# Kernel optimization log

Measured on AMD Instinct MI355X. Metric: run time of the kernel, lower is better.

## Reference

```python
import jax, jax.numpy as jnp
import numpy as np
from jax import lax

B, C, H, W = 8, 256, 32, 32
HEADS = 8
NUM_OFF = 9
OFF_SCALE = 0.1


def setup_inputs() -> dict:
    key = jax.random.key(0)
    ks = jax.random.split(key, 8)
    f = lambda k, s, sc: jax.random.normal(k, s, dtype=jnp.float32) * sc
    return {
        'query_map': f(ks[0], (B, C, H, W), 1.0),
        'kv_map': f(ks[1], (B, C, H, W), 1.0),
        'Wq': f(ks[2], (C, C), C ** -0.5),
        'Wk': f(ks[3], (C, C), C ** -0.5),
        'Wv': f(ks[4], (C, C), C ** -0.5),
        'Woff1': f(ks[5], (C // 2, C, 3, 3), (C * 9) ** -0.5),
        'boff1': jnp.zeros((C // 2,), jnp.float32),
        'Woff2': f(ks[6], (NUM_OFF * 2, C // 2), (C // 2) ** -0.5),
        'boff2': jnp.zeros((NUM_OFF * 2,), jnp.float32),
        'Wout': f(ks[7], (C, C), C ** -0.5),
        'bout': jnp.zeros((C,), jnp.float32),
    }


def grid_sample_bilinear_border(img, grid):
    """img: (B,C,H,W); grid: (B,H,W,2) with (x,y) in [-1,1], align_corners=True,
    padding_mode='border'. Returns (B,C,H,W)."""
    Bn, Cn, Hn, Wn = img.shape
    x = (grid[..., 0] + 1.0) * 0.5 * (Wn - 1)
    y = (grid[..., 1] + 1.0) * 0.5 * (Hn - 1)
    # border padding: clamp continuous coords into the valid range
    x = jnp.clip(x, 0.0, Wn - 1)
    y = jnp.clip(y, 0.0, Hn - 1)
    x0 = jnp.floor(x)
    y0 = jnp.floor(y)
    wx = x - x0
    wy = y - y0
    x0i = x0.astype(jnp.int32)
    y0i = y0.astype(jnp.int32)
    x1i = jnp.minimum(x0i + 1, Wn - 1)
    y1i = jnp.minimum(y0i + 1, Hn - 1)
    flat = img.reshape(Bn, Cn, Hn * Wn)

    def gat(iy, ix):
        idx = (iy * Wn + ix).reshape(Bn, 1, -1)  # broadcasts over channels
        return jnp.take_along_axis(flat, idx, axis=2)

    v00 = gat(y0i, x0i)
    v01 = gat(y0i, x1i)
    v10 = gat(y1i, x0i)
    v11 = gat(y1i, x1i)
    wxf = wx.reshape(Bn, 1, -1)
    wyf = wy.reshape(Bn, 1, -1)
    out = (v00 * (1 - wxf) + v01 * wxf) * (1 - wyf) + (v10 * (1 - wxf) + v11 * wxf) * wyf
    return out.reshape(Bn, Cn, Hn, Wn)


def reference(query_map, kv_map, Wq, Wk, Wv, Woff1, boff1, Woff2, boff2, Wout, bout):
    Bn, Cn, Hn, Wn = query_map.shape
    hd = Cn // HEADS
    # 1x1 conv projections as channel einsums
    q = jnp.einsum('oc,bchw->bohw', Wq, query_map)
    # offset network: 3x3 conv -> relu -> 1x1 conv
    h1 = lax.conv_general_dilated(q, Woff1, (1, 1), 'SAME',
                                  dimension_numbers=('NCHW', 'OIHW', 'NCHW'))
    h1 = jax.nn.relu(h1 + boff1[None, :, None, None])
    offsets = jnp.einsum('oc,bchw->bohw', Woff2, h1) + boff2[None, :, None, None]
    offsets = offsets.reshape(Bn, NUM_OFF, 2, Hn, Wn)
    offset = offsets[:, 0] * OFF_SCALE  # (B,2,H,W); ch0 -> x, ch1 -> y
    # normalized base grid in [-1,1] (align_corners=True convention)
    gx = jnp.linspace(-1.0, 1.0, Wn, dtype=q.dtype)[None, :]  # (1,W)
    gy = jnp.linspace(-1.0, 1.0, Hn, dtype=q.dtype)[:, None]  # (H,1)
    vx = gx[None] + offset[:, 0]  # (B,H,W)
    vy = gy[None] + offset[:, 1]
    vgrid = jnp.stack([vx, vy], axis=-1)  # (B,H,W,2)
    kv_sampled = grid_sample_bilinear_border(kv_map, vgrid)
    k = jnp.einsum('oc,bchw->bohw', Wk, kv_sampled)
    v = jnp.einsum('oc,bchw->bohw', Wv, kv_sampled)
    # (B,C,H,W) -> (B,heads,HW,hd)
    def to_heads(t):
        return t.reshape(Bn, HEADS, hd, Hn * Wn).transpose(0, 1, 3, 2)
    qh, kh, vh = to_heads(q), to_heads(k), to_heads(v)
    scale = hd ** -0.5
    attn = jnp.einsum('bhqd,bhkd->bhqk', qh, kh) * scale
    attn = jax.nn.softmax(attn, axis=-1)
    out = jnp.einsum('bhqk,bhkd->bhqd', attn, vh)
    out = out.transpose(0, 1, 3, 2).reshape(Bn, Cn, Hn, Wn)
    out = jnp.einsum('oc,bchw->bohw', Wout, out) + bout[None, :, None, None]
    return out
```

## Files before the change

kernel.cpp:

```cpp
#include <hip/hip_runtime.h>

#define HW_ 1024

typedef __attribute__((ext_vector_type(8))) short bf16x8;
typedef __attribute__((ext_vector_type(4))) short bf16x4;
typedef __attribute__((ext_vector_type(4))) float f32x4;

__device__ inline unsigned short f2bf(float f) {
  unsigned int u = __float_as_uint(f);
  u += 0x7FFF + ((u >> 16) & 1);
  return (unsigned short)(u >> 16);
}
__device__ inline unsigned short f2bf_fast(float f) {
  return (unsigned short)((__float_as_uint(f) + 0x8000u) >> 16);
}
__device__ inline float bf2f(unsigned short h) {
  return __uint_as_float(((unsigned int)h) << 16);
}
__device__ inline void async_copy16(const void* g, void* l) {
  __builtin_amdgcn_global_load_lds(
      (const __attribute__((address_space(1))) unsigned int*)g,
      (__attribute__((address_space(3))) unsigned int*)l, 16, 0, 0);
}

__global__ __launch_bounds__(256) void prep(
    const float* __restrict__ kv,
    const float* __restrict__ Wq, const float* __restrict__ Wk,
    const float* __restrict__ Wv, const float* __restrict__ Wo,
    const float* __restrict__ Woff1,
    short* __restrict__ WH, short* __restrict__ WL, short* __restrict__ wb,
    float* __restrict__ kvT)
{
  __shared__ float T[256][33];
  const int bid = blockIdx.x, t = threadIdx.x;

  if (bid < 256) {
    int b = bid >> 5, p0 = (bid & 31) * 32;
    int pp = t & 31, cg = t >> 5;
#pragma unroll
    for (int i = 0; i < 32; ++i) {
      int c = cg * 32 + i;
      T[c][pp] = kv[((size_t)(b * 256 + c)) * HW_ + p0 + pp];
    }
    __syncthreads();
#pragma unroll
    for (int r = 0; r < 8; ++r) {
      int e = t + 256 * r;
      int c4 = (e & 63) * 4, pp2 = e >> 6;
      float4 v4;
      v4.x = T[c4 + 0][pp2];
      v4.y = T[c4 + 1][pp2];
      v4.z = T[c4 + 2][pp2];
      v4.w = T[c4 + 3][pp2];
      *(float4*)&kvT[((size_t)(b * 1024 + p0 + pp2)) * 256 + c4] = v4;
    }
  } else if (bid < 512) {
    int b2 = bid - 256;
    int mat = b2 >> 6;
    int loc = (b2 & 63) * 1024 + t * 4;
    const float* W = (mat == 0) ? Wq : (mat == 1) ? Wk : (mat == 2) ? Wv : Wo;
    float4 f4 = *(const float4*)&W[loc];
    float f[4] = {f4.x, f4.y, f4.z, f4.w};
    bf16x4 h4, l4;
#pragma unroll
    for (int j = 0; j < 4; ++j) {
      unsigned short h = f2bf(f[j]);
      h4[j] = (short)h;
      l4[j] = (short)f2bf(f[j] - bf2f(h));
    }
    int r = loc >> 8, c = loc & 255;
    int mtile = r >> 4, k0s = c >> 5;
    int lane_ = ((c >> 3) & 3) * 16 + (r & 15);
    int pidx = (((mtile * 8 + k0s) * 64 + lane_) * 8) + (c & 7);
    *(bf16x4*)&WH[mat * 65536 + pidx] = h4;
    *(bf16x4*)&WL[mat * 65536 + pidx] = l4;
  } else {
    int e0 = (bid - 512) * 1024 + t * 4;
    int c = e0 & 255;
    int o = (e0 >> 8) & 127;
    int tap = e0 >> 15;
    bf16x4 h4;
#pragma unroll
    for (int j = 0; j < 4; ++j)
      h4[j] = (short)f2bf(Woff1[((size_t)(o * 256 + c + j)) * 9 + tap]);
    int otile = o >> 4, c0s = c >> 5;
    int lane_ = ((c >> 3) & 3) * 16 + (o & 15);
    int widx = ((((tap * 8 + otile) * 8 + c0s) * 64 + lane_) * 8) + (c & 7);
    *(bf16x4*)&wb[widx] = h4;
  }
}

__global__ __launch_bounds__(256) void qgemm(
    const short* __restrict__ WH, const short* __restrict__ WL,
    const float* __restrict__ Xf,
    short* __restrict__ Yt, short* __restrict__ Yh2, short* __restrict__ Yl2)
{
  __shared__ short Bsh[32][40];
  __shared__ short Bsl[32][40];
  const int t    = threadIdx.x;
  const int w    = t >> 6;
  const int lane = t & 63;
  const int ln   = lane & 15;
  const int qd   = lane >> 4;
  const int bp0  = blockIdx.x * 32;
  const int mb   = blockIdx.y * 8 + w * 2;
  const int bB   = bp0 >> 10, p0l = bp0 & 1023;

  f32x4 acc[2][2] = {};
#pragma unroll
  for (int k0 = 0; k0 < 256; k0 += 32) {
    __syncthreads();
    {
      int pp = t & 31, cg = t >> 5;
      float fv[4];
#pragma unroll
      for (int j = 0; j < 4; ++j)
        fv[j] = Xf[((size_t)(bB * 256 + k0 + cg * 4 + j)) * HW_ + p0l + pp];
      bf16x4 h4, l4;
#pragma unroll
      for (int j = 0; j < 4; ++j) {
        unsigned short h = f2bf(fv[j]);
        h4[j] = (short)h;
        l4[j] = (short)f2bf(fv[j] - bf2f(h));
      }
      *(bf16x4*)&Bsh[pp][cg * 4] = h4;
      *(bf16x4*)&Bsl[pp][cg * 4] = l4;
    }
    __syncthreads();

    bf16x8 Ah[2], Al[2], Bh[2], Bl[2];
    const int k0s = k0 >> 5;
#pragma unroll
    for (int mt = 0; mt < 2; ++mt) {
      size_t wi = ((size_t)(((mb + mt) * 8 + k0s) * 64 + lane)) * 8;
      Ah[mt] = *(const bf16x8*)&WH[wi];
      Al[mt] = *(const bf16x8*)&WL[wi];
    }
#pragma unroll
    for (int nt = 0; nt < 2; ++nt) {
      Bh[nt] = *(const bf16x8*)&Bsh[nt * 16 + ln][qd * 8];
      Bl[nt] = *(const bf16x8*)&Bsl[nt * 16 + ln][qd * 8];
    }
#pragma unroll
    for (int mt = 0; mt < 2; ++mt)
#pragma unroll
      for (int nt = 0; nt < 2; ++nt) {
        acc[mt][nt] = __builtin_amdgcn_mfma_f32_16x16x32_bf16(Ah[mt], Bh[nt], acc[mt][nt], 0, 0, 0);
        acc[mt][nt] = __builtin_amdgcn_mfma_f32_16x16x32_bf16(Ah[mt], Bl[nt], acc[mt][nt], 0, 0, 0);
        acc[mt][nt] = __builtin_amdgcn_mfma_f32_16x16x32_bf16(Al[mt], Bh[nt], acc[mt][nt], 0, 0, 0);
      }
  }

  const int om = blockIdx.y * 128 + w * 32;
  const float sc = 0.25506063286f;
#pragma unroll
  for (int mt = 0; mt < 2; ++mt)
#pragma unroll
    for (int nt = 0; nt < 2; ++nt) {
      int bp = bp0 + nt * 16 + ln;
      int b = bp >> 10, p = bp & 1023;
#pragma unroll
      for (int i = 0; i < 4; ++i) {
        int o = om + mt * 16 + qd * 4 + i;
        int h = o >> 5, d = o & 31;
        Yt[(((size_t)(b * 8 + h)) * 1024 + p) * 32 + d] = (short)f2bf(acc[mt][nt][i] * sc);
      }
      int ob = om + mt * 16 + qd * 4;
      bf16x4 h4, l4;
#pragma unroll
      for (int i = 0; i < 4; ++i) {
        float f = acc[mt][nt][i];
        unsigned short h = f2bf(f);
        h4[i] = (short)h;
        l4[i] = (short)f2bf(f - bf2f(h));
      }
      *(bf16x4*)&Yh2[(size_t)bp * 256 + ob] = h4;
      *(bf16x4*)&Yl2[(size_t)bp * 256 + ob] = l4;
    }
}

__global__ __launch_bounds__(512) void convkv(
    const short* __restrict__ wb, const float* __restrict__ bias,
    const float* __restrict__ W2, const float* __restrict__ b2,
    const short* __restrict__ xh, const short* __restrict__ xl,
    const float* __restrict__ kvT,
    const short* __restrict__ WH, const short* __restrict__ WL,
    short* __restrict__ kt, short* __restrict__ vt)
{
  __shared__ short Xs[2][3][34][264];
  __shared__ short XsH[32][264];
  __shared__ short XsL[32][264];
  __shared__ float red[4][32][2];
  __shared__ float2 crd[32];
  const int id   = blockIdx.x;
  const int b    = id & 7;
  const int y0   = id >> 3;
  const int t    = threadIdx.x;
  const int w    = t >> 6;
  const int lane = t & 63;
  const int ln   = lane & 15;
  const int qd   = lane >> 4;
  const int bp0  = (b * 32 + y0) * 32;

  {
    bf16x8 v[12];
#pragma unroll
    for (int i = 0; i < 12; ++i) {
      int e = t + 512 * i;
      int oct = e & 31;
      int x   = (e >> 5) & 31;
      int rr  = e >> 10;
      int hl  = rr / 3, r = rr % 3;
      int yy  = y0 + r - 1;
      bf16x8 val = {};
      if (yy >= 0 && yy < 32) {
        const short* src = hl ? xl : xh;
        val = *(const bf16x8*)&src[((size_t)((b * 32 + yy) * 32 + x)) * 256 + oct * 8];
      }
      v[i] = val;
    }
#pragma unroll
    for (int i = 0; i < 12; ++i) {
      int e = t + 512 * i;
      int oct = e & 31;
      int x   = (e >> 5) & 31;
      int rr  = e >> 10;
      int hl  = rr / 3, r = rr % 3;
      *(bf16x8*)&Xs[hl][r][x + 1][oct * 8] = v[i];
    }
    if (t < 384) {
      int oct  = t & 31;
      int colw = (t >> 5) & 1;
      int rr   = t >> 6;
      int hl   = rr / 3, r = rr % 3;
      bf16x8 zz = {};
      *(bf16x8*)&Xs[hl][r][colw ? 33 : 0][oct * 8] = zz;
    }
  }
  __syncthreads();

  const int chh = w >> 2;
  const int ow  = w & 3;
  const int o0c = ow * 32;
  f32x4 acc[2][2] = {};
#pragma unroll
  for (int c0s = 0; c0s < 4; ++c0s) {
    const int c0 = chh * 128 + c0s * 32;
    const int c0abs = chh * 4 + c0s;
#pragma unroll
    for (int tap = 0; tap < 9; ++tap) {
      const int ky = tap / 3, kx = tap % 3;
      bf16x8 afr[2];
#pragma unroll
      for (int m = 0; m < 2; ++m)
        afr[m] = *(const bf16x8*)&wb[((((tap * 8 + (ow * 2 + m)) * 8 + c0abs) * 64
                                       + lane) * 8)];
#pragma unroll
      for (int nt = 0; nt < 2; ++nt) {
        int hc = nt * 16 + ln + kx;
        bf16x8 bh = *(const bf16x8*)&Xs[0][ky][hc][c0 + qd * 8];
        bf16x8 bl = *(const bf16x8*)&Xs[1][ky][hc][c0 + qd * 8];
#pragma unroll
        for (int m = 0; m < 2; ++m) {
          acc[m][nt] = __builtin_amdgcn_mfma_f32_16x16x32_bf16(afr[m], bh, acc[m][nt], 0, 0, 0);
          acc[m][nt] = __builtin_amdgcn_mfma_f32_16x16x32_bf16(afr[m], bl, acc[m][nt], 0, 0, 0);
        }
      }
    }
  }

  float* ps = (float*)&XsH[0][0];
  if (w >= 4) {
#pragma unroll
    for (int m = 0; m < 2; ++m)
#pragma unroll
      for (int nt = 0; nt < 2; ++nt)
        *(f32x4*)&ps[(((w - 4) * 64 + lane) * 4 + m * 2 + nt) * 4] = acc[m][nt];
  }
  __syncthreads();

  if (w < 4) {
    float ps0[2] = {0.f, 0.f}, ps1[2] = {0.f, 0.f};
#pragma unroll
    for (int m = 0; m < 2; ++m)
#pragma unroll
      for (int nt = 0; nt < 2; ++nt) {
        f32x4 p = *(const f32x4*)&ps[((w * 64 + lane) * 4 + m * 2 + nt) * 4];
        acc[m][nt] += p;
      }
#pragma unroll
    for (int m = 0; m < 2; ++m)
#pragma unroll
      for (int i = 0; i < 4; ++i) {
        int o = o0c + m * 16 + qd * 4 + i;
        float bo = bias[o];
        float w2a = W2[o], w2b = W2[128 + o];
#pragma unroll
        for (int nt = 0; nt < 2; ++nt) {
          float h = fmaxf(acc[m][nt][i] + bo, 0.f);
          ps0[nt] += w2a * h;
          ps1[nt] += w2b * h;
        }
      }
#pragma unroll
    for (int msk = 16; msk < 64; msk <<= 1) {
      ps0[0] += __shfl_xor(ps0[0], msk, 64);
      ps0[1] += __shfl_xor(ps0[1], msk, 64);
      ps1[0] += __shfl_xor(ps1[0], msk, 64);
      ps1[1] += __shfl_xor(ps1[1], msk, 64);
    }
    if (qd == 0) {
#pragma unroll
      for (int nt = 0; nt < 2; ++nt) {
        red[w][nt * 16 + ln][0] = ps0[nt];
        red[w][nt * 16 + ln][1] = ps1[nt];
      }
    }
  }
  __syncthreads();
  if (t < 32) {
    float c0s = (red[0][t][0] + red[1][t][0]) + (red[2][t][0] + red[3][t][0]) + b2[0];
    float c1s = (red[0][t][1] + red[1][t][1]) + (red[2][t][1] + red[3][t][1]) + b2[1];
    float gx = -1.f + 2.f * (float)t / 31.f;
    float gy = -1.f + 2.f * (float)y0 / 31.f;
    float vx = gx + 0.1f * c0s;
    float vy = gy + 0.1f * c1s;
    float px = fminf(fmaxf((vx + 1.f) * 0.5f * 31.f, 0.f), 31.f);
    float py = fminf(fmaxf((vy + 1.f) * 0.5f * 31.f, 0.f), 31.f);
    crd[t] = make_float2(px, py);
  }
  __syncthreads();

#pragma unroll
  for (int it = 0; it < 2; ++it) {
    int e = t + 512 * it;
    int oct = e & 31, row = e >> 5;
    float2 cd = crd[row];
    float x0f = floorf(cd.x), y0f = floorf(cd.y);
    float wx = cd.x - x0f, wy = cd.y - y0f;
    int x0 = (int)x0f, y0i = (int)y0f;
    int x1 = min(x0 + 1, 31), y1 = min(y0i + 1, 31);
    float w00 = (1.f - wx) * (1.f - wy), w01 = wx * (1.f - wy);
    float w10 = (1.f - wx) * wy,         w11 = wx * wy;
    const float* r00 = &kvT[((size_t)(b * 1024 + y0i * 32 + x0)) * 256 + oct * 8];
    const float* r01 = &kvT[((size_t)(b * 1024 + y0i * 32 + x1)) * 256 + oct * 8];
    const float* r10 = &kvT[((size_t)(b * 1024 + y1 * 32 + x0)) * 256 + oct * 8];
    const float* r11 = &kvT[((size_t)(b * 1024 + y1 * 32 + x1)) * 256 + oct * 8];
    float4 a00 = *(const float4*)r00, b00 = *(const float4*)(r00 + 4);
    float4 a01 = *(const float4*)r01, b01 = *(const float4*)(r01 + 4);
    float4 a10 = *(const float4*)r10, b10 = *(const float4*)(r10 + 4);
    float4 a11 = *(const float4*)r11, b11 = *(const float4*)(r11 + 4);
    float v[8];
    v[0] = a00.x * w00 + a01.x * w01 + a10.x * w10 + a11.x * w11;
    v[1] = a00.y * w00 + a01.y * w01 + a10.y * w10 + a11.y * w11;
    v[2] = a00.z * w00 + a01.z * w01 + a10.z * w10 + a11.z * w11;
    v[3] = a00.w * w00 + a01.w * w01 + a10.w * w10 + a11.w * w11;
    v[4] = b00.x * w00 + b01.x * w01 + b10.x * w10 + b11.x * w11;
    v[5] = b00.y * w00 + b01.y * w01 + b10.y * w10 + b11.y * w11;
    v[6] = b00.z * w00 + b01.z * w01 + b10.z * w10 + b11.z * w11;
    v[7] = b00.w * w00 + b01.w * w01 + b10.w * w10 + b11.w * w11;
    bf16x8 h8, l8;
#pragma unroll
    for (int j = 0; j < 8; ++j) {
      unsigned short h = f2bf(v[j]);
      h8[j] = (short)h;
      l8[j] = (short)f2bf(v[j] - bf2f(h));
    }
    *(bf16x8*)&XsH[row][oct * 8] = h8;
    *(bf16x8*)&XsL[row][oct * 8] = l8;
  }
  __syncthreads();

  const int mat  = w >> 2;
  const short* WAh = WH + (mat ? 131072 : 65536);
  const short* WAl = WL + (mat ? 131072 : 65536);
  const int om4 = (w & 3) * 4;

  f32x4 acg[4][2] = {};
#pragma unroll
  for (int k0 = 0; k0 < 256; k0 += 32) {
    const int k0s = k0 >> 5;
    bf16x8 Bh[2], Bl[2];
#pragma unroll
    for (int nt = 0; nt < 2; ++nt) {
      Bh[nt] = *(const bf16x8*)&XsH[nt * 16 + ln][k0 + qd * 8];
      Bl[nt] = *(const bf16x8*)&XsL[nt * 16 + ln][k0 + qd * 8];
    }
#pragma unroll
    for (int mt = 0; mt < 4; ++mt) {
      size_t wi = ((size_t)(((om4 + mt) * 8 + k0s) * 64 + lane)) * 8;
      bf16x8 Ah = *(const bf16x8*)&WAh[wi];
      bf16x8 Al = *(const bf16x8*)&WAl[wi];
#pragma unroll
      for (int nt = 0; nt < 2; ++nt) {
        acg[mt][nt] = __builtin_amdgcn_mfma_f32_16x16x32_bf16(Ah, Bh[nt], acg[mt][nt], 0, 0, 0);
        acg[mt][nt] = __builtin_amdgcn_mfma_f32_16x16x32_bf16(Ah, Bl[nt], acg[mt][nt], 0, 0, 0);
        acg[mt][nt] = __builtin_amdgcn_mfma_f32_16x16x32_bf16(Al, Bh[nt], acg[mt][nt], 0, 0, 0);
      }
    }
  }

#pragma unroll
  for (int mt = 0; mt < 4; ++mt)
#pragma unroll
    for (int nt = 0; nt < 2; ++nt) {
      int p  = bp0 + nt * 16 + ln;
      int pl = p & 1023;
      int jt = pl >> 6, jl = pl & 63;
#pragma unroll
      for (int i = 0; i < 4; ++i) {
        int oc = (w & 3) * 64 + mt * 16 + qd * 4 + i;
        unsigned short val = f2bf(acg[mt][nt][i]);
        int bhead = b * 8 + (oc >> 5), d = oc & 31;
        if (mat == 0) {
          int cd2 = (d >> 3) ^ ((jl >> 2) & 3);
          kt[((((size_t)(bhead * 16 + jt)) * 64 + jl) * 4 + cd2) * 8 + (d & 7)] = (short)val;
        } else {
          int jjs = ((jl & 15) << 2) | (jl >> 4);
          int cj = (jjs >> 3) ^ (d & 7);
          vt[((((size_t)(bhead * 16 + jt)) * 32 + d) * 8 + cj) * 8 + (jjs & 7)] = (short)val;
        }
      }
    }
}

__global__ __launch_bounds__(256) void attn_mfma(
    const short* __restrict__ qt, const short* __restrict__ kt,
    const short* __restrict__ vt, short* __restrict__ aoh,
    short* __restrict__ aol)
{
  __shared__ __align__(16) short Ks[2][2048];
  __shared__ __align__(16) short Vs[2][2048];
  __shared__ __align__(16) short P[4][32][72];
  const int t    = threadIdx.x;
  const int w    = t >> 6;
  const int lane = t & 63;
  const int ln   = lane & 15;
  const int qd   = lane >> 4;
  const int id   = blockIdx.x;
  const int b    = id & 7;
  const int rem  = id >> 3;
  const int h    = rem & 7;
  const int qc   = rem >> 3;
  const int bh   = b * 8 + h;
  const int qbase = qc * 128 + w * 16;

  const short* ktb = kt + (size_t)bh * 32768;
  const short* vtb = vt + (size_t)bh * 32768;

  bf16x8 aq[2];
  aq[0] = *(const bf16x8*)&qt[((size_t)(bh * 1024 + qbase + ln)) * 32 + qd * 8];
  aq[1] = *(const bf16x8*)&qt[((size_t)(bh * 1024 + qbase + 64 + ln)) * 32 + qd * 8];

  f32x4 acc[2][2] = {};
  float lacc[2][4] = {};
  const f32x4 zero = {0.f, 0.f, 0.f, 0.f};

  const int stoff = w * 512 + lane * 8;
  const int ldoff = w * 512;

  async_copy16(&ktb[stoff], &Ks[0][ldoff]);
  async_copy16(&vtb[stoff], &Vs[0][ldoff]);
  __syncthreads();

  for (int jt = 0; jt < 16; ++jt) {
    const int cur = jt & 1, nxt = cur ^ 1;
    if (jt < 15) {
      async_copy16(&ktb[(jt + 1) * 2048 + stoff], &Ks[nxt][ldoff]);
      async_copy16(&vtb[(jt + 1) * 2048 + stoff], &Vs[nxt][ldoff]);
    }

    bf16x8 bk[4], bv[2][2];
#pragma unroll
    for (int kk = 0; kk < 4; ++kk)
      bk[kk] = *(const bf16x8*)&Ks[cur][((kk * 16 + ln) * 4 + (qd ^ ((ln >> 2) & 3))) * 8];
#pragma unroll
    for (int kc = 0; kc < 2; ++kc)
#pragma unroll
      for (int ds = 0; ds < 2; ++ds)
        bv[kc][ds] = *(const bf16x8*)&Vs[cur][((ds * 16 + ln) * 8 + ((kc * 4 + qd) ^ (ln & 7))) * 8];

#pragma unroll
    for (int qf = 0; qf < 2; ++qf) {
      f32x4 s[4];
      __builtin_amdgcn_s_setprio(1);
#pragma unroll
      for (int kk = 0; kk < 4; ++kk)
        s[kk] = __builtin_amdgcn_mfma_f32_16x16x32_bf16(aq[qf], bk[kk], zero, 0, 0, 0);
      __builtin_amdgcn_s_setprio(0);

#pragma unroll
      for (int i = 0; i < 4; ++i) {
        float p0 = __builtin_amdgcn_exp2f(s[0][i]);
        float p1 = __builtin_amdgcn_exp2f(s[1][i]);
        float p2 = __builtin_amdgcn_exp2f(s[2][i]);
        float p3 = __builtin_amdgcn_exp2f(s[3][i]);
        s[0][i] = p0; s[1][i] = p1; s[2][i] = p2; s[3][i] = p3;
        lacc[qf][i] += (p0 + p1) + (p2 + p3);
      }
#pragma unroll
      for (int i = 0; i < 4; ++i) {
        bf16x4 p4;
#pragma unroll
        for (int kk = 0; kk < 4; ++kk) p4[kk] = (short)f2bf_fast(s[kk][i]);
        *(bf16x4*)&P[w][qf * 16 + qd * 4 + i][4 * ln] = p4;
      }
      __builtin_amdgcn_s_setprio(1);
#pragma unroll
      for (int kc = 0; kc < 2; ++kc) {
        bf16x8 ap = *(const bf16x8*)&P[w][qf * 16 + ln][kc * 32 + qd * 8];
#pragma unroll
        for (int ds = 0; ds < 2; ++ds)
          acc[qf][ds] = __builtin_amdgcn_mfma_f32_16x16x32_bf16(ap, bv[kc][ds], acc[qf][ds], 0, 0, 0);
      }
      __builtin_amdgcn_s_setprio(0);
    }

    __syncthreads();
  }

  const int bb = bh >> 3, hh2 = bh & 7;
#pragma unroll
  for (int qf = 0; qf < 2; ++qf)
#pragma unroll
    for (int i = 0; i < 4; ++i) {
      float l = lacc[qf][i];
      l += __shfl_xor(l, 1, 64);
      l += __shfl_xor(l, 2, 64);
      l += __shfl_xor(l, 4, 64);
      l += __shfl_xor(l, 8, 64);
      float inv = 1.f / l;
      int qrow = qbase + qf * 64 + qd * 4 + i;
#pragma unroll
      for (int ds = 0; ds < 2; ++ds) {
        float v = acc[qf][ds][i] * inv;
        unsigned short hv = f2bf(v);
        size_t idx = ((size_t)(bb * 1024 + qrow)) * 256 + hh2 * 32 + ds * 16 + ln;
        aoh[idx] = (short)hv;
        aol[idx] = (short)f2bf(v - bf2f(hv));
      }
    }
}

__global__ __launch_bounds__(256) void gemm_out(
    const short* __restrict__ Wh, const short* __restrict__ Wl,
    const short* __restrict__ Xh, const short* __restrict__ Xl,
    const float* __restrict__ bias, float* __restrict__ Yf)
{
  __shared__ short XsH[32][264];
  __shared__ short XsL[32][264];
  const int t    = threadIdx.x;
  const int w    = t >> 6;
  const int lane = t & 63;
  const int ln   = lane & 15;
  const int qd   = lane >> 4;
  const int bp0  = blockIdx.x * 32;
  const int mb   = blockIdx.y * 8 + w * 2;

#pragma unroll
  for (int it = 0; it < 4; ++it) {
    int e = t + 256 * it;
    int oct = e & 31, row = e >> 5;
    bf16x8 vh = *(const bf16x8*)&Xh[((size_t)(bp0 + row)) * 256 + oct * 8];
    bf16x8 vl = *(const bf16x8*)&Xl[((size_t)(bp0 + row)) * 256 + oct * 8];
    *(bf16x8*)&XsH[row][oct * 8] = vh;
    *(bf16x8*)&XsL[row][oct * 8] = vl;
  }
  __syncthreads();

  f32x4 acc[2][2] = {};
#pragma unroll
  for (int k0 = 0; k0 < 256; k0 += 32) {
    const int k0s = k0 >> 5;
    bf16x8 Ah[2], Al[2], Bh[2], Bl[2];
#pragma unroll
    for (int mt = 0; mt < 2; ++mt) {
      size_t wi = ((size_t)(((mb + mt) * 8 + k0s) * 64 + lane)) * 8;
      Ah[mt] = *(const bf16x8*)&Wh[wi];
      Al[mt] = *(const bf16x8*)&Wl[wi];
    }
#pragma unroll
    for (int nt = 0; nt < 2; ++nt) {
      Bh[nt] = *(const bf16x8*)&XsH[nt * 16 + ln][k0 + qd * 8];
      Bl[nt] = *(const bf16x8*)&XsL[nt * 16 + ln][k0 + qd * 8];
    }
#pragma unroll
    for (int mt = 0; mt < 2; ++mt)
#pragma unroll
      for (int nt = 0; nt < 2; ++nt) {
        acc[mt][nt] = __builtin_amdgcn_mfma_f32_16x16x32_bf16(Ah[mt], Bh[nt], acc[mt][nt], 0, 0, 0);
        acc[mt][nt] = __builtin_amdgcn_mfma_f32_16x16x32_bf16(Ah[mt], Bl[nt], acc[mt][nt], 0, 0, 0);
        acc[mt][nt] = __builtin_amdgcn_mfma_f32_16x16x32_bf16(Al[mt], Bh[nt], acc[mt][nt], 0, 0, 0);
      }
  }

  const int om = blockIdx.y * 128 + w * 32;
#pragma unroll
  for (int mt = 0; mt < 2; ++mt)
#pragma unroll
    for (int i = 0; i < 4; ++i) {
      int o = om + mt * 16 + qd * 4 + i;
      float bo = bias[o];
#pragma unroll
      for (int nt = 0; nt < 2; ++nt) {
        int bp = bp0 + nt * 16 + ln;
        int b = bp >> 10, p = bp & 1023;
        Yf[((size_t)(b * 256 + o)) * HW_ + p] = acc[mt][nt][i] + bo;
      }
    }
}

extern "C" void kernel_launch(void* const* d_in, const int* in_sizes, int n_in,
                              void* d_out, int out_size, void* d_ws, size_t ws_size,
                              hipStream_t stream)
{
  const float* query_map = (const float*)d_in[0];
  const float* kv_map    = (const float*)d_in[1];
  const float* Wq        = (const float*)d_in[2];
  const float* Wk        = (const float*)d_in[3];
  const float* Wv        = (const float*)d_in[4];
  const float* Woff1     = (const float*)d_in[5];
  const float* boff1     = (const float*)d_in[6];
  const float* Woff2     = (const float*)d_in[7];
  const float* boff2     = (const float*)d_in[8];
  const float* Wout      = (const float*)d_in[9];
  const float* bout      = (const float*)d_in[10];
  float* out = (float*)d_out;
  char* base = (char*)d_ws;

  const size_t MB = 1u << 20;
  short* qt     = (short*)(base + 1 * MB);
  short* kt     = (short*)(base + 5 * MB);
  short* vt     = (short*)(base + 9 * MB);
  short* bufBh  = (short*)(base + 13 * MB);
  short* bufBl  = (short*)(base + 17 * MB);
  short* wb     = (short*)(base + 21 * MB);
  short* WH     = (short*)(base + 22 * MB);
  short* WL     = (short*)(base + 23 * MB);
  float* kvT    = (float*)(base + 24 * MB);

  prep<<<dim3(800), dim3(256), 0, stream>>>(kv_map, Wq, Wk, Wv, Wout, Woff1,
                                            WH, WL, wb, kvT);
  qgemm<<<dim3(256, 2), dim3(256), 0, stream>>>(WH, WL, query_map,
                                                qt, bufBh, bufBl);
  convkv<<<dim3(256), dim3(512), 0, stream>>>(wb, boff1, Woff2, boff2,
                                              bufBh, bufBl, kvT, WH, WL, kt, vt);
  attn_mfma<<<dim3(512), dim3(256), 0, stream>>>(qt, kt, vt, bufBh, bufBl);
  gemm_out<<<dim3(256, 2), dim3(256), 0, stream>>>(WH + 196608, WL + 196608,
                                                   bufBh, bufBl, bout, out);
}
```

Before: 161.9 us.

## Fuse all five stages into one cooperative persistent kernel with grid syncs

```diff
diff --git a/kernel.cpp b/kernel.cpp
--- a/kernel.cpp
+++ b/kernel.cpp
@@ -1,4 +1,7 @@
 #include <hip/hip_runtime.h>
+#include <hip/hip_cooperative_groups.h>
+
+namespace cg = cooperative_groups;
 
 #define HW_ 1024
 
@@ -23,29 +26,42 @@
       (__attribute__((address_space(3))) unsigned int*)l, 16, 0, 0);
 }
 
-__global__ __launch_bounds__(256) void prep(
+__global__ __launch_bounds__(512) void mega(
     const float* __restrict__ kv,
     const float* __restrict__ Wq, const float* __restrict__ Wk,
     const float* __restrict__ Wv, const float* __restrict__ Wo,
-    const float* __restrict__ Woff1,
+    const float* __restrict__ Woff1, const float* __restrict__ boff1,
+    const float* __restrict__ Woff2, const float* __restrict__ boff2,
+    const float* __restrict__ bout, const float* __restrict__ Xf,
+    float* __restrict__ out,
     short* __restrict__ WH, short* __restrict__ WL, short* __restrict__ wb,
-    float* __restrict__ kvT)
+    float* __restrict__ kvT, short* __restrict__ qt,
+    short* __restrict__ kt, short* __restrict__ vt,
+    short* __restrict__ bufBh, short* __restrict__ bufBl)
 {
-  __shared__ float T[256][33];
-  const int bid = blockIdx.x, t = threadIdx.x;
-
-  if (bid < 256) {
+  __shared__ __align__(16) char SM[142784];
+  cg::grid_group grid = cg::this_grid();
+
+  const int bid  = blockIdx.x;
+  const int t    = threadIdx.x;
+  const int w    = t >> 6;
+  const int lane = t & 63;
+  const int ln   = lane & 15;
+  const int qd   = lane >> 4;
+
+  {
+    auto T = (float (*)[33])SM;
     int b = bid >> 5, p0 = (bid & 31) * 32;
-    int pp = t & 31, cg = t >> 5;
-#pragma unroll
-    for (int i = 0; i < 32; ++i) {
-      int c = cg * 32 + i;
+    int pp = t & 31, cg16 = t >> 5;
+#pragma unroll
+    for (int i = 0; i < 16; ++i) {
+      int c = cg16 * 16 + i;
       T[c][pp] = kv[((size_t)(b * 256 + c)) * HW_ + p0 + pp];
     }
     __syncthreads();
 #pragma unroll
-    for (int r = 0; r < 8; ++r) {
-      int e = t + 256 * r;
+    for (int r = 0; r < 4; ++r) {
+      int e = t + 512 * r;
       int c4 = (e & 63) * 4, pp2 = e >> 6;
       float4 v4;
       v4.x = T[c4 + 0][pp2];
@@ -54,560 +70,533 @@
       v4.w = T[c4 + 3][pp2];
       *(float4*)&kvT[((size_t)(b * 1024 + p0 + pp2)) * 256 + c4] = v4;
     }
-  } else if (bid < 512) {
-    int b2 = bid - 256;
-    int mat = b2 >> 6;
-    int loc = (b2 & 63) * 1024 + t * 4;
-    const float* W = (mat == 0) ? Wq : (mat == 1) ? Wk : (mat == 2) ? Wv : Wo;
-    float4 f4 = *(const float4*)&W[loc];
-    float f[4] = {f4.x, f4.y, f4.z, f4.w};
-    bf16x4 h4, l4;
-#pragma unroll
-    for (int j = 0; j < 4; ++j) {
-      unsigned short h = f2bf(f[j]);
-      h4[j] = (short)h;
-      l4[j] = (short)f2bf(f[j] - bf2f(h));
-    }
-    int r = loc >> 8, c = loc & 255;
-    int mtile = r >> 4, k0s = c >> 5;
-    int lane_ = ((c >> 3) & 3) * 16 + (r & 15);
-    int pidx = (((mtile * 8 + k0s) * 64 + lane_) * 8) + (c & 7);
-    *(bf16x4*)&WH[mat * 65536 + pidx] = h4;
-    *(bf16x4*)&WL[mat * 65536 + pidx] = l4;
-  } else {
-    int e0 = (bid - 512) * 1024 + t * 4;
-    int c = e0 & 255;
-    int o = (e0 >> 8) & 127;
-    int tap = e0 >> 15;
-    bf16x4 h4;
-#pragma unroll
-    for (int j = 0; j < 4; ++j)
-      h4[j] = (short)f2bf(Woff1[((size_t)(o * 256 + c + j)) * 9 + tap]);
-    int otile = o >> 4, c0s = c >> 5;
-    int lane_ = ((c >> 3) & 3) * 16 + (o & 15);
-    int widx = ((((tap * 8 + otile) * 8 + c0s) * 64 + lane_) * 8) + (c & 7);
-    *(bf16x4*)&wb[widx] = h4;
+    if (t < 256) {
+      int lg = bid * 1024 + t * 4;
+      int mat = lg >> 16;
+      int loc = lg & 65535;
+      const float* W = (mat == 0) ? Wq : (mat == 1) ? Wk : (mat == 2) ? Wv : Wo;
+      float4 f4 = *(const float4*)&W[loc];
+      float f[4] = {f4.x, f4.y, f4.z, f4.w};
+      bf16x4 h4, l4;
+#pragma unroll
+      for (int j = 0; j < 4; ++j) {
+        unsigned short h = f2bf(f[j]);
+        h4[j] = (short)h;
+        l4[j] = (short)f2bf(f[j] - bf2f(h));
+      }
+      int r = loc >> 8, c = loc & 255;
+      int mtile = r >> 4, k0s = c >> 5;
+      int lane_ = ((c >> 3) & 3) * 16 + (r & 15);
+      int pidx = (((mtile * 8 + k0s) * 64 + lane_) * 8) + (c & 7);
+      *(bf16x4*)&WH[mat * 65536 + pidx] = h4;
+      *(bf16x4*)&WL[mat * 65536 + pidx] = l4;
+    }
+    if (t < 288) {
+      int e0 = bid * 1152 + t * 4;
+      int c = e0 & 255;
+      int o = (e0 >> 8) & 127;
+      int tap = e0 >> 15;
+      bf16x4 h4;
+#pragma unroll
+      for (int j = 0; j < 4; ++j)
+        h4[j] = (short)f2bf(Woff1[((size_t)(o * 256 + c + j)) * 9 + tap]);
+      int otile = o >> 4, c0s = c >> 5;
+      int lane_ = ((c >> 3) & 3) * 16 + (o & 15);
+      int widx = ((((tap * 8 + otile) * 8 + c0s) * 64 + lane_) * 8) + (c & 7);
+      *(bf16x4*)&wb[widx] = h4;
+    }
   }
-}
-
-__global__ __launch_bounds__(256) void qgemm(
-    const short* __restrict__ WH, const short* __restrict__ WL,
-    const float* __restrict__ Xf,
-    short* __restrict__ Yt, short* __restrict__ Yh2, short* __restrict__ Yl2)
-{
-  __shared__ short Bsh[32][40];
-  __shared__ short Bsl[32][40];
-  const int t    = threadIdx.x;
-  const int w    = t >> 6;
-  const int lane = t & 63;
-  const int ln   = lane & 15;
-  const int qd   = lane >> 4;
-  const int bp0  = blockIdx.x * 32;
-  const int mb   = blockIdx.y * 8 + w * 2;
-  const int bB   = bp0 >> 10, p0l = bp0 & 1023;
-
-  f32x4 acc[2][2] = {};
-#pragma unroll
-  for (int k0 = 0; k0 < 256; k0 += 32) {
-    __syncthreads();
+  grid.sync();
+
+  {
+    auto Bsh = (short (*)[264])(SM);
+    auto Bsl = (short (*)[264])(SM + 16896);
+    const int bp0 = bid * 32;
+    const int bB = bp0 >> 10, p0l = bp0 & 1023;
     {
-      int pp = t & 31, cg = t >> 5;
-      float fv[4];
-#pragma unroll
-      for (int j = 0; j < 4; ++j)
-        fv[j] = Xf[((size_t)(bB * 256 + k0 + cg * 4 + j)) * HW_ + p0l + pp];
-      bf16x4 h4, l4;
-#pragma unroll
-      for (int j = 0; j < 4; ++j) {
-        unsigned short h = f2bf(fv[j]);
-        h4[j] = (short)h;
-        l4[j] = (short)f2bf(fv[j] - bf2f(h));
-      }
-      *(bf16x4*)&Bsh[pp][cg * 4] = h4;
-      *(bf16x4*)&Bsl[pp][cg * 4] = l4;
-    }
-    __syncthreads();
-
-    bf16x8 Ah[2], Al[2], Bh[2], Bl[2];
-    const int k0s = k0 >> 5;
-#pragma unroll
-    for (int mt = 0; mt < 2; ++mt) {
-      size_t wi = ((size_t)(((mb + mt) * 8 + k0s) * 64 + lane)) * 8;
-      Ah[mt] = *(const bf16x8*)&WH[wi];
-      Al[mt] = *(const bf16x8*)&WL[wi];
-    }
-#pragma unroll
-    for (int nt = 0; nt < 2; ++nt) {
-      Bh[nt] = *(const bf16x8*)&Bsh[nt * 16 + ln][qd * 8];
-      Bl[nt] = *(const bf16x8*)&Bsl[nt * 16 + ln][qd * 8];
-    }
+      int pp = t & 31, cs = t >> 5;
+      float fv[16];
+#pragma unroll
+      for (int j = 0; j < 16; ++j)
+        fv[j] = Xf[((size_t)(bB * 256 + cs * 16 + j)) * HW_ + p0l + pp];
+#pragma unroll
+      for (int g = 0; g < 4; ++g) {
+        bf16x4 h4, l4;
+#pragma unroll
+        for (int j = 0; j < 4; ++j) {
+          float f = fv[g * 4 + j];
+          unsigned short h = f2bf(f);
+          h4[j] = (short)h;
+          l4[j] = (short)f2bf(f - bf2f(h));
+        }
+        *(bf16x4*)&Bsh[pp][cs * 16 + g * 4] = h4;
+        *(bf16x4*)&Bsl[pp][cs * 16 + g * 4] = l4;
+      }
+    }
+    __syncthreads();
+
+    const int mh = w >> 2, ww = w & 3;
+    const int mb = mh * 8 + ww * 2;
+    f32x4 acc[2][2] = {};
+#pragma unroll
+    for (int k0 = 0; k0 < 256; k0 += 32) {
+      const int k0s = k0 >> 5;
+      bf16x8 Ah[2], Al[2], Bh[2], Bl[2];
+#pragma unroll
+      for (int mt = 0; mt < 2; ++mt) {
+        size_t wi = ((size_t)(((mb + mt) * 8 + k0s) * 64 + lane)) * 8;
+        Ah[mt] = *(const bf16x8*)&WH[wi];
+        Al[mt] = *(const bf16x8*)&WL[wi];
+      }
+#pragma unroll
+      for (int nt = 0; nt < 2; ++nt) {
+        Bh[nt] = *(const bf16x8*)&Bsh[nt * 16 + ln][k0 + qd * 8];
+        Bl[nt] = *(const bf16x8*)&Bsl[nt * 16 + ln][k0 + qd * 8];
+      }
+#pragma unroll
+      for (int mt = 0; mt < 2; ++mt)
+#pragma unroll
+        for (int nt = 0; nt < 2; ++nt) {
+          acc[mt][nt] = __builtin_amdgcn_mfma_f32_16x16x32_bf16(Ah[mt], Bh[nt], acc[mt][nt], 0, 0, 0);
+          acc[mt][nt] = __builtin_amdgcn_mfma_f32_16x16x32_bf16(Ah[mt], Bl[nt], acc[mt][nt], 0, 0, 0);
+          acc[mt][nt] = __builtin_amdgcn_mfma_f32_16x16x32_bf16(Al[mt], Bh[nt], acc[mt][nt], 0, 0, 0);
+        }
+    }
+
+    const int om = mh * 128 + ww * 32;
+    const float sc = 0.25506063286f;
 #pragma unroll
     for (int mt = 0; mt < 2; ++mt)
-#pragma unroll
-      for (int nt = 0; nt < 2; ++nt) {
-        acc[mt][nt] = __builtin_amdgcn_mfma_f32_16x16x32_bf16(Ah[mt], Bh[nt], acc[mt][nt], 0, 0, 0);
-        acc[mt][nt] = __builtin_amdgcn_mfma_f32_16x16x32_bf16(Ah[mt], Bl[nt], acc[mt][nt], 0, 0, 0);
-        acc[mt][nt] = __builtin_amdgcn_mfma_f32_16x16x32_bf16(Al[mt], Bh[nt], acc[mt][nt], 0, 0, 0);
-      }
-  }
-
-  const int om = blockIdx.y * 128 + w * 32;
-  const float sc = 0.25506063286f;
-#pragma unroll
-  for (int mt = 0; mt < 2; ++mt)
-#pragma unroll
-    for (int nt = 0; nt < 2; ++nt) {
-      int bp = bp0 + nt * 16 + ln;
-      int b = bp >> 10, p = bp & 1023;
-#pragma unroll
-      for (int i = 0; i < 4; ++i) {
-        int o = om + mt * 16 + qd * 4 + i;
-        int h = o >> 5, d = o & 31;
-        Yt[(((size_t)(b * 8 + h)) * 1024 + p) * 32 + d] = (short)f2bf(acc[mt][nt][i] * sc);
-      }
-      int ob = om + mt * 16 + qd * 4;
-      bf16x4 h4, l4;
-#pragma unroll
-      for (int i = 0; i < 4; ++i) {
-        float f = acc[mt][nt][i];
-        unsigned short h = f2bf(f);
-        h4[i] = (short)h;
-        l4[i] = (short)f2bf(f - bf2f(h));
-      }
-      *(bf16x4*)&Yh2[(size_t)bp * 256 + ob] = h4;
-      *(bf16x4*)&Yl2[(size_t)bp * 256 + ob] = l4;
-    }
-}
-
-__global__ __launch_bounds__(512) void convkv(
-    const short* __restrict__ wb, const float* __restrict__ bias,
-    const float* __restrict__ W2, const float* __restrict__ b2,
-    const short* __restrict__ xh, const short* __restrict__ xl,
-    const float* __restrict__ kvT,
-    const short* __restrict__ WH, const short* __restrict__ WL,
-    short* __restrict__ kt, short* __restrict__ vt)
-{
-  __shared__ short Xs[2][3][34][264];
-  __shared__ short XsH[32][264];
-  __shared__ short XsL[32][264];
-  __shared__ float red[4][32][2];
-  __shared__ float2 crd[32];
-  const int id   = blockIdx.x;
-  const int b    = id & 7;
-  const int y0   = id >> 3;
-  const int t    = threadIdx.x;
-  const int w    = t >> 6;
-  const int lane = t & 63;
-  const int ln   = lane & 15;
-  const int qd   = lane >> 4;
-  const int bp0  = (b * 32 + y0) * 32;
-
-  {
-    bf16x8 v[12];
-#pragma unroll
-    for (int i = 0; i < 12; ++i) {
-      int e = t + 512 * i;
-      int oct = e & 31;
-      int x   = (e >> 5) & 31;
-      int rr  = e >> 10;
-      int hl  = rr / 3, r = rr % 3;
-      int yy  = y0 + r - 1;
-      bf16x8 val = {};
-      if (yy >= 0 && yy < 32) {
-        const short* src = hl ? xl : xh;
-        val = *(const bf16x8*)&src[((size_t)((b * 32 + yy) * 32 + x)) * 256 + oct * 8];
-      }
-      v[i] = val;
-    }
-#pragma unroll
-    for (int i = 0; i < 12; ++i) {
-      int e = t + 512 * i;
-      int oct = e & 31;
-      int x   = (e >> 5) & 31;
-      int rr  = e >> 10;
-      int hl  = rr / 3, r = rr % 3;
-      *(bf16x8*)&Xs[hl][r][x + 1][oct * 8] = v[i];
-    }
-    if (t < 384) {
-      int oct  = t & 31;
-      int colw = (t >> 5) & 1;
-      int rr   = t >> 6;
-      int hl   = rr / 3, r = rr % 3;
-      bf16x8 zz = {};
-      *(bf16x8*)&Xs[hl][r][colw ? 33 : 0][oct * 8] = zz;
-    }
-  }
-  __syncthreads();
-
-  const int chh = w >> 2;
-  const int ow  = w & 3;
-  const int o0c = ow * 32;
-  f32x4 acc[2][2] = {};
-#pragma unroll
-  for (int c0s = 0; c0s < 4; ++c0s) {
-    const int c0 = chh * 128 + c0s * 32;
-    const int c0abs = chh * 4 + c0s;
-#pragma unroll
-    for (int tap = 0; tap < 9; ++tap) {
-      const int ky = tap / 3, kx = tap % 3;
-      bf16x8 afr[2];
-#pragma unroll
-      for (int m = 0; m < 2; ++m)
-        afr[m] = *(const bf16x8*)&wb[((((tap * 8 + (ow * 2 + m)) * 8 + c0abs) * 64
-                                       + lane) * 8)];
-#pragma unroll
-      for (int nt = 0; nt < 2; ++nt) {
-        int hc = nt * 16 + ln + kx;
-        bf16x8 bh = *(const bf16x8*)&Xs[0][ky][hc][c0 + qd * 8];
-        bf16x8 bl = *(const bf16x8*)&Xs[1][ky][hc][c0 + qd * 8];
-#pragma unroll
-        for (int m = 0; m < 2; ++m) {
-          acc[m][nt] = __builtin_amdgcn_mfma_f32_16x16x32_bf16(afr[m], bh, acc[m][nt], 0, 0, 0);
-          acc[m][nt] = __builtin_amdgcn_mfma_f32_16x16x32_bf16(afr[m], bl, acc[m][nt], 0, 0, 0);
-        }
-      }
-    }
-  }
-
-  float* ps = (float*)&XsH[0][0];
-  if (w >= 4) {
-#pragma unroll
-    for (int m = 0; m < 2; ++m)
-#pragma unroll
-      for (int nt = 0; nt < 2; ++nt)
-        *(f32x4*)&ps[(((w - 4) * 64 + lane) * 4 + m * 2 + nt) * 4] = acc[m][nt];
-  }
-  __syncthreads();
-
-  if (w < 4) {
-    float ps0[2] = {0.f, 0.f}, ps1[2] = {0.f, 0.f};
-#pragma unroll
-    for (int m = 0; m < 2; ++m)
-#pragma unroll
-      for (int nt = 0; nt < 2; ++nt) {
-        f32x4 p = *(const f32x4*)&ps[((w * 64 + lane) * 4 + m * 2 + nt) * 4];
-        acc[m][nt] += p;
-      }
-#pragma unroll
-    for (int m = 0; m < 2; ++m)
-#pragma unroll
-      for (int i = 0; i < 4; ++i) {
-        int o = o0c + m * 16 + qd * 4 + i;
-        float bo = bias[o];
-        float w2a = W2[o], w2b = W2[128 + o];
-#pragma unroll
-        for (int nt = 0; nt < 2; ++nt) {
-          float h = fmaxf(acc[m][nt][i] + bo, 0.f);
-          ps0[nt] += w2a * h;
-          ps1[nt] += w2b * h;
-        }
-      }
-#pragma unroll
-    for (int msk = 16; msk < 64; msk <<= 1) {
-      ps0[0] += __shfl_xor(ps0[0], msk, 64);
-      ps0[1] += __shfl_xor(ps0[1], msk, 64);
-      ps1[0] += __shfl_xor(ps1[0], msk, 64);
-      ps1[1] += __shfl_xor(ps1[1], msk, 64);
-    }
-    if (qd == 0) {
-#pragma unroll
-      for (int nt = 0; nt < 2; ++nt) {
-        red[w][nt * 16 + ln][0] = ps0[nt];
-        red[w][nt * 16 + ln][1] = ps1[nt];
-      }
-    }
-  }
-  __syncthreads();
-  if (t < 32) {
-    float c0s = (red[0][t][0] + red[1][t][0]) + (red[2][t][0] + red[3][t][0]) + b2[0];
-    float c1s = (red[0][t][1] + red[1][t][1]) + (red[2][t][1] + red[3][t][1]) + b2[1];
-    float gx = -1.f + 2.f * (float)t / 31.f;
-    float gy = -1.f + 2.f * (float)y0 / 31.f;
-    float vx = gx + 0.1f * c0s;
-    float vy = gy + 0.1f * c1s;
-    float px = fminf(fmaxf((vx + 1.f) * 0.5f * 31.f, 0.f), 31.f);
-    float py = fminf(fmaxf((vy + 1.f) * 0.5f * 31.f, 0.f), 31.f);
-    crd[t] = make_float2(px, py);
-  }
-  __syncthreads();
-
-#pragma unroll
-  for (int it = 0; it < 2; ++it) {
-    int e = t + 512 * it;
-    int oct = e & 31, row = e >> 5;
-    float2 cd = crd[row];
-    float x0f = floorf(cd.x), y0f = floorf(cd.y);
-    float wx = cd.x - x0f, wy = cd.y - y0f;
-    int x0 = (int)x0f, y0i = (int)y0f;
-    int x1 = min(x0 + 1, 31), y1 = min(y0i + 1, 31);
-    float w00 = (1.f - wx) * (1.f - wy), w01 = wx * (1.f - wy);
-    float w10 = (1.f - wx) * wy,         w11 = wx * wy;
-    const float* r00 = &kvT[((size_t)(b * 1024 + y0i * 32 + x0)) * 256 + oct * 8];
-    const float* r01 = &kvT[((size_t)(b * 1024 + y0i * 32 + x1)) * 256 + oct * 8];
-    const float* r10 = &kvT[((size_t)(b * 1024 + y1 * 32 + x0)) * 256 + oct * 8];
-    const float* r11 = &kvT[((size_t)(b * 1024 + y1 * 32 + x1)) * 256 + oct * 8];
-    float4 a00 = *(const float4*)r00, b00 = *(const float4*)(r00 + 4);
-    float4 a01 = *(const float4*)r01, b01 = *(const float4*)(r01 + 4);
-    float4 a10 = *(const float4*)r10, b10 = *(const float4*)(r10 + 4);
-    float4 a11 = *(const float4*)r11, b11 = *(const float4*)(r11 + 4);
-    float v[8];
-    v[0] = a00.x * w00 + a01.x * w01 + a10.x * w10 + a11.x * w11;
-    v[1] = a00.y * w00 + a01.y * w01 + a10.y * w10 + a11.y * w11;
-    v[2] = a00.z * w00 + a01.z * w01 + a10.z * w10 + a11.z * w11;
-    v[3] = a00.w * w00 + a01.w * w01 + a10.w * w10 + a11.w * w11;
-    v[4] = b00.x * w00 + b01.x * w01 + b10.x * w10 + b11.x * w11;
-    v[5] = b00.y * w00 + b01.y * w01 + b10.y * w10 + b11.y * w11;
-    v[6] = b00.z * w00 + b01.z * w01 + b10.z * w10 + b11.z * w11;
-    v[7] = b00.w * w00 + b01.w * w01 + b10.w * w10 + b11.w * w11;
-    bf16x8 h8, l8;
-#pragma unroll
-    for (int j = 0; j < 8; ++j) {
-      unsigned short h = f2bf(v[j]);
-      h8[j] = (short)h;
-      l8[j] = (short)f2bf(v[j] - bf2f(h));
-    }
-    *(bf16x8*)&XsH[row][oct * 8] = h8;
-    *(bf16x8*)&XsL[row][oct * 8] = l8;
-  }
-  __syncthreads();
-
-  const int mat  = w >> 2;
-  const short* WAh = WH + (mat ? 131072 : 65536);
-  const short* WAl = WL + (mat ? 131072 : 65536);
-  const int om4 = (w & 3) * 4;
-
-  f32x4 acg[4][2] = {};
-#pragma unroll
-  for (int k0 = 0; k0 < 256; k0 += 32) {
-    const int k0s = k0 >> 5;
-    bf16x8 Bh[2], Bl[2];
-#pragma unroll
-    for (int nt = 0; nt < 2; ++nt) {
-      Bh[nt] = *(const bf16x8*)&XsH[nt * 16 + ln][k0 + qd * 8];
-      Bl[nt] = *(const bf16x8*)&XsL[nt * 16 + ln][k0 + qd * 8];
-    }
-#pragma unroll
-    for (int mt = 0; mt < 4; ++mt) {
-      size_t wi = ((size_t)(((om4 + mt) * 8 + k0s) * 64 + lane)) * 8;
-      bf16x8 Ah = *(const bf16x8*)&WAh[wi];
-      bf16x8 Al = *(const bf16x8*)&WAl[wi];
-#pragma unroll
-      for (int nt = 0; nt < 2; ++nt) {
-        acg[mt][nt] = __builtin_amdgcn_mfma_f32_16x16x32_bf16(Ah, Bh[nt], acg[mt][nt], 0, 0, 0);
-        acg[mt][nt] = __builtin_amdgcn_mfma_f32_16x16x32_bf16(Ah, Bl[nt], acg[mt][nt], 0, 0, 0);
-        acg[mt][nt] = __builtin_amdgcn_mfma_f32_16x16x32_bf16(Al, Bh[nt], acg[mt][nt], 0, 0, 0);
-      }
-    }
-  }
-
-#pragma unroll
-  for (int mt = 0; mt < 4; ++mt)
-#pragma unroll
-    for (int nt = 0; nt < 2; ++nt) {
-      int p  = bp0 + nt * 16 + ln;
-      int pl = p & 1023;
-      int jt = pl >> 6, jl = pl & 63;
-#pragma unroll
-      for (int i = 0; i < 4; ++i) {
-        int oc = (w & 3) * 64 + mt * 16 + qd * 4 + i;
-        unsigned short val = f2bf(acg[mt][nt][i]);
-        int bhead = b * 8 + (oc >> 5), d = oc & 31;
-        if (mat == 0) {
-          int cd2 = (d >> 3) ^ ((jl >> 2) & 3);
-          kt[((((size_t)(bhead * 16 + jt)) * 64 + jl) * 4 + cd2) * 8 + (d & 7)] = (short)val;
-        } else {
-          int jjs = ((jl & 15) << 2) | (jl >> 4);
-          int cj = (jjs >> 3) ^ (d & 7);
-          vt[((((size_t)(bhead * 16 + jt)) * 32 + d) * 8 + cj) * 8 + (jjs & 7)] = (short)val;
-        }
-      }
-    }
-}
-
-__global__ __launch_bounds__(256) void attn_mfma(
-    const short* __restrict__ qt, const short* __restrict__ kt,
-    const short* __restrict__ vt, short* __restrict__ aoh,
-    short* __restrict__ aol)
-{
-  __shared__ __align__(16) short Ks[2][2048];
-  __shared__ __align__(16) short Vs[2][2048];
-  __shared__ __align__(16) short P[4][32][72];
-  const int t    = threadIdx.x;
-  const int w    = t >> 6;
-  const int lane = t & 63;
-  const int ln   = lane & 15;
-  const int qd   = lane >> 4;
-  const int id   = blockIdx.x;
-  const int b    = id & 7;
-  const int rem  = id >> 3;
-  const int h    = rem & 7;
-  const int qc   = rem >> 3;
-  const int bh   = b * 8 + h;
-  const int qbase = qc * 128 + w * 16;
-
-  const short* ktb = kt + (size_t)bh * 32768;
-  const short* vtb = vt + (size_t)bh * 32768;
-
-  bf16x8 aq[2];
-  aq[0] = *(const bf16x8*)&qt[((size_t)(bh * 1024 + qbase + ln)) * 32 + qd * 8];
-  aq[1] = *(const bf16x8*)&qt[((size_t)(bh * 1024 + qbase + 64 + ln)) * 32 + qd * 8];
-
-  f32x4 acc[2][2] = {};
-  float lacc[2][4] = {};
-  const f32x4 zero = {0.f, 0.f, 0.f, 0.f};
-
-  const int stoff = w * 512 + lane * 8;
-  const int ldoff = w * 512;
-
-  async_copy16(&ktb[stoff], &Ks[0][ldoff]);
-  async_copy16(&vtb[stoff], &Vs[0][ldoff]);
-  __syncthreads();
-
-  for (int jt = 0; jt < 16; ++jt) {
-    const int cur = jt & 1, nxt = cur ^ 1;
-    if (jt < 15) {
-      async_copy16(&ktb[(jt + 1) * 2048 + stoff], &Ks[nxt][ldoff]);
-      async_copy16(&vtb[(jt + 1) * 2048 + stoff], &Vs[nxt][ldoff]);
-    }
-
-    bf16x8 bk[4], bv[2][2];
-#pragma unroll
-    for (int kk = 0; kk < 4; ++kk)
-      bk[kk] = *(const bf16x8*)&Ks[cur][((kk * 16 + ln) * 4 + (qd ^ ((ln >> 2) & 3))) * 8];
-#pragma unroll
-    for (int kc = 0; kc < 2; ++kc)
-#pragma unroll
-      for (int ds = 0; ds < 2; ++ds)
-        bv[kc][ds] = *(const bf16x8*)&Vs[cur][((ds * 16 + ln) * 8 + ((kc * 4 + qd) ^ (ln & 7))) * 8];
-
-#pragma unroll
-    for (int qf = 0; qf < 2; ++qf) {
-      f32x4 s[4];
-      __builtin_amdgcn_s_setprio(1);
-#pragma unroll
-      for (int kk = 0; kk < 4; ++kk)
-        s[kk] = __builtin_amdgcn_mfma_f32_16x16x32_bf16(aq[qf], bk[kk], zero, 0, 0, 0);
-      __builtin_amdgcn_s_setprio(0);
-
-#pragma unroll
-      for (int i = 0; i < 4; ++i) {
-        float p0 = __builtin_amdgcn_exp2f(s[0][i]);
-        float p1 = __builtin_amdgcn_exp2f(s[1][i]);
-        float p2 = __builtin_amdgcn_exp2f(s[2][i]);
-        float p3 = __builtin_amdgcn_exp2f(s[3][i]);
-        s[0][i] = p0; s[1][i] = p1; s[2][i] = p2; s[3][i] = p3;
-        lacc[qf][i] += (p0 + p1) + (p2 + p3);
-      }
-#pragma unroll
-      for (int i = 0; i < 4; ++i) {
-        bf16x4 p4;
-#pragma unroll
-        for (int kk = 0; kk < 4; ++kk) p4[kk] = (short)f2bf_fast(s[kk][i]);
-        *(bf16x4*)&P[w][qf * 16 + qd * 4 + i][4 * ln] = p4;
-      }
-      __builtin_amdgcn_s_setprio(1);
-#pragma unroll
-      for (int kc = 0; kc < 2; ++kc) {
-        bf16x8 ap = *(const bf16x8*)&P[w][qf * 16 + ln][kc * 32 + qd * 8];
-#pragma unroll
-        for (int ds = 0; ds < 2; ++ds)
-          acc[qf][ds] = __builtin_amdgcn_mfma_f32_16x16x32_bf16(ap, bv[kc][ds], acc[qf][ds], 0, 0, 0);
-      }
-      __builtin_amdgcn_s_setprio(0);
-    }
-
-    __syncthreads();
-  }
-
-  const int bb = bh >> 3, hh2 = bh & 7;
-#pragma unroll
-  for (int qf = 0; qf < 2; ++qf)
-#pragma unroll
-    for (int i = 0; i < 4; ++i) {
-      float l = lacc[qf][i];
-      l += __shfl_xor(l, 1, 64);
-      l += __shfl_xor(l, 2, 64);
-      l += __shfl_xor(l, 4, 64);
-      l += __shfl_xor(l, 8, 64);
-      float inv = 1.f / l;
-      int qrow = qbase + qf * 64 + qd * 4 + i;
-#pragma unroll
-      for (int ds = 0; ds < 2; ++ds) {
-        float v = acc[qf][ds][i] * inv;
-        unsigned short hv = f2bf(v);
-        size_t idx = ((size_t)(bb * 1024 + qrow)) * 256 + hh2 * 32 + ds * 16 + ln;
-        aoh[idx] = (short)hv;
-        aol[idx] = (short)f2bf(v - bf2f(hv));
-      }
-    }
-}
-
-__global__ __launch_bounds__(256) void gemm_out(
-    const short* __restrict__ Wh, const short* __restrict__ Wl,
-    const short* __restrict__ Xh, const short* __restrict__ Xl,
-    const float* __restrict__ bias, float* __restrict__ Yf)
-{
-  __shared__ short XsH[32][264];
-  __shared__ short XsL[32][264];
-  const int t    = threadIdx.x;
-  const int w    = t >> 6;
-  const int lane = t & 63;
-  const int ln   = lane & 15;
-  const int qd   = lane >> 4;
-  const int bp0  = blockIdx.x * 32;
-  const int mb   = blockIdx.y * 8 + w * 2;
-
-#pragma unroll
-  for (int it = 0; it < 4; ++it) {
-    int e = t + 256 * it;
-    int oct = e & 31, row = e >> 5;
-    bf16x8 vh = *(const bf16x8*)&Xh[((size_t)(bp0 + row)) * 256 + oct * 8];
-    bf16x8 vl = *(const bf16x8*)&Xl[((size_t)(bp0 + row)) * 256 + oct * 8];
-    *(bf16x8*)&XsH[row][oct * 8] = vh;
-    *(bf16x8*)&XsL[row][oct * 8] = vl;
-  }
-  __syncthreads();
-
-  f32x4 acc[2][2] = {};
-#pragma unroll
-  for (int k0 = 0; k0 < 256; k0 += 32) {
-    const int k0s = k0 >> 5;
-    bf16x8 Ah[2], Al[2], Bh[2], Bl[2];
-#pragma unroll
-    for (int mt = 0; mt < 2; ++mt) {
-      size_t wi = ((size_t)(((mb + mt) * 8 + k0s) * 64 + lane)) * 8;
-      Ah[mt] = *(const bf16x8*)&Wh[wi];
-      Al[mt] = *(const bf16x8*)&Wl[wi];
-    }
-#pragma unroll
-    for (int nt = 0; nt < 2; ++nt) {
-      Bh[nt] = *(const bf16x8*)&XsH[nt * 16 + ln][k0 + qd * 8];
-      Bl[nt] = *(const bf16x8*)&XsL[nt * 16 + ln][k0 + qd * 8];
-    }
-#pragma unroll
-    for (int mt = 0; mt < 2; ++mt)
-#pragma unroll
-      for (int nt = 0; nt < 2; ++nt) {
-        acc[mt][nt] = __builtin_amdgcn_mfma_f32_16x16x32_bf16(Ah[mt], Bh[nt], acc[mt][nt], 0, 0, 0);
-        acc[mt][nt] = __builtin_amdgcn_mfma_f32_16x16x32_bf16(Ah[mt], Bl[nt], acc[mt][nt], 0, 0, 0);
-        acc[mt][nt] = __builtin_amdgcn_mfma_f32_16x16x32_bf16(Al[mt], Bh[nt], acc[mt][nt], 0, 0, 0);
-      }
-  }
-
-  const int om = blockIdx.y * 128 + w * 32;
-#pragma unroll
-  for (int mt = 0; mt < 2; ++mt)
-#pragma unroll
-    for (int i = 0; i < 4; ++i) {
-      int o = om + mt * 16 + qd * 4 + i;
-      float bo = bias[o];
 #pragma unroll
       for (int nt = 0; nt < 2; ++nt) {
         int bp = bp0 + nt * 16 + ln;
         int b = bp >> 10, p = bp & 1023;
-        Yf[((size_t)(b * 256 + o)) * HW_ + p] = acc[mt][nt][i] + bo;
-      }
-    }
+#pragma unroll
+        for (int i = 0; i < 4; ++i) {
+          int o = om + mt * 16 + qd * 4 + i;
+          int h = o >> 5, d = o & 31;
+          qt[(((size_t)(b * 8 + h)) * 1024 + p) * 32 + d] = (short)f2bf(acc[mt][nt][i] * sc);
+        }
+        int ob = om + mt * 16 + qd * 4;
+        bf16x4 h4, l4;
+#pragma unroll
+        for (int i = 0; i < 4; ++i) {
+          float f = acc[mt][nt][i];
+          unsigned short h = f2bf(f);
+          h4[i] = (short)h;
+          l4[i] = (short)f2bf(f - bf2f(h));
+        }
+        *(bf16x4*)&bufBh[(size_t)bp * 256 + ob] = h4;
+        *(bf16x4*)&bufBl[(size_t)bp * 256 + ob] = l4;
+      }
+  }
+  grid.sync();
+
+  {
+    auto Xs  = (short (*)[3][34][264])(SM);
+    auto XsH = (short (*)[264])(SM + 107712);
+    auto XsL = (short (*)[264])(SM + 124608);
+    auto red = (float (*)[32][2])(SM + 141504);
+    auto crd = (float2*)(SM + 142528);
+    const int b  = bid & 7;
+    const int y0 = bid >> 3;
+    const int bp0 = (b * 32 + y0) * 32;
+
+    {
+      bf16x8 v[12];
+#pragma unroll
+      for (int i = 0; i < 12; ++i) {
+        int e = t + 512 * i;
+        int oct = e & 31;
+        int x   = (e >> 5) & 31;
+        int rr  = e >> 10;
+        int hl  = rr / 3, r = rr % 3;
+        int yy  = y0 + r - 1;
+        bf16x8 val = {};
+        if (yy >= 0 && yy < 32) {
+          const short* src = hl ? bufBl : bufBh;
+          val = *(const bf16x8*)&src[((size_t)((b * 32 + yy) * 32 + x)) * 256 + oct * 8];
+        }
+        v[i] = val;
+      }
+#pragma unroll
+      for (int i = 0; i < 12; ++i) {
+        int e = t + 512 * i;
+        int oct = e & 31;
+        int x   = (e >> 5) & 31;
+        int rr  = e >> 10;
+        int hl  = rr / 3, r = rr % 3;
+        *(bf16x8*)&Xs[hl][r][x + 1][oct * 8] = v[i];
+      }
+      if (t < 384) {
+        int oct  = t & 31;
+        int colw = (t >> 5) & 1;
+        int rr   = t >> 6;
+        int hl   = rr / 3, r = rr % 3;
+        bf16x8 zz = {};
+        *(bf16x8*)&Xs[hl][r][colw ? 33 : 0][oct * 8] = zz;
+      }
+    }
+    __syncthreads();
+
+    const int chh = w >> 2;
+    const int ow  = w & 3;
+    const int o0c = ow * 32;
+    f32x4 acc[2][2] = {};
+#pragma unroll
+    for (int c0s = 0; c0s < 4; ++c0s) {
+      const int c0 = chh * 128 + c0s * 32;
+      const int c0abs = chh * 4 + c0s;
+#pragma unroll
+      for (int tap = 0; tap < 9; ++tap) {
+        const int ky = tap / 3, kx = tap % 3;
+        bf16x8 afr[2];
+#pragma unroll
+        for (int m = 0; m < 2; ++m)
+          afr[m] = *(const bf16x8*)&wb[((((tap * 8 + (ow * 2 + m)) * 8 + c0abs) * 64
+                                         + lane) * 8)];
+#pragma unroll
+        for (int nt = 0; nt < 2; ++nt) {
+          int hc = nt * 16 + ln + kx;
+          bf16x8 bh = *(const bf16x8*)&Xs[0][ky][hc][c0 + qd * 8];
+          bf16x8 bl = *(const bf16x8*)&Xs[1][ky][hc][c0 + qd * 8];
+#pragma unroll
+          for (int m = 0; m < 2; ++m) {
+            acc[m][nt] = __builtin_amdgcn_mfma_f32_16x16x32_bf16(afr[m], bh, acc[m][nt], 0, 0, 0);
+            acc[m][nt] = __builtin_amdgcn_mfma_f32_16x16x32_bf16(afr[m], bl, acc[m][nt], 0, 0, 0);
+          }
+        }
+      }
+    }
+
+    float* ps = (float*)&XsH[0][0];
+    if (w >= 4) {
+#pragma unroll
+      for (int m = 0; m < 2; ++m)
+#pragma unroll
+        for (int nt = 0; nt < 2; ++nt)
+          *(f32x4*)&ps[(((w - 4) * 64 + lane) * 4 + m * 2 + nt) * 4] = acc[m][nt];
+    }
+    __syncthreads();
+
+    if (w < 4) {
+      float ps0[2] = {0.f, 0.f}, ps1[2] = {0.f, 0.f};
+#pragma unroll
+      for (int m = 0; m < 2; ++m)
+#pragma unroll
+        for (int nt = 0; nt < 2; ++nt) {
+          f32x4 p = *(const f32x4*)&ps[((w * 64 + lane) * 4 + m * 2 + nt) * 4];
+          acc[m][nt] += p;
+        }
+#pragma unroll
+      for (int m = 0; m < 2; ++m)
+#pragma unroll
+        for (int i = 0; i < 4; ++i) {
+          int o = o0c + m * 16 + qd * 4 + i;
+          float bo = boff1[o];
+          float w2a = Woff2[o], w2b = Woff2[128 + o];
+#pragma unroll
+          for (int nt = 0; nt < 2; ++nt) {
+            float h = fmaxf(acc[m][nt][i] + bo, 0.f);
+            ps0[nt] += w2a * h;
+            ps1[nt] += w2b * h;
+          }
+        }
+#pragma unroll
+      for (int msk = 16; msk < 64; msk <<= 1) {
+        ps0[0] += __shfl_xor(ps0[0], msk, 64);
+        ps0[1] += __shfl_xor(ps0[1], msk, 64);
+        ps1[0] += __shfl_xor(ps1[0], msk, 64);
+        ps1[1] += __shfl_xor(ps1[1], msk, 64);
+      }
+      if (qd == 0) {
+#pragma unroll
+        for (int nt = 0; nt < 2; ++nt) {
+          red[w][nt * 16 + ln][0] = ps0[nt];
+          red[w][nt * 16 + ln][1] = ps1[nt];
+        }
+      }
+    }
+    __syncthreads();
+    if (t < 32) {
+      float c0s = (red[0][t][0] + red[1][t][0]) + (red[2][t][0] + red[3][t][0]) + boff2[0];
+      float c1s = (red[0][t][1] + red[1][t][1]) + (red[2][t][1] + red[3][t][1]) + boff2[1];
+      float gx = -1.f + 2.f * (float)t / 31.f;
+      float gy = -1.f + 2.f * (float)y0 / 31.f;
+      float vx = gx + 0.1f * c0s;
+      float vy = gy + 0.1f * c1s;
+      float px = fminf(fmaxf((vx + 1.f) * 0.5f * 31.f, 0.f), 31.f);
+      float py = fminf(fmaxf((vy + 1.f) * 0.5f * 31.f, 0.f), 31.f);
+      crd[t] = make_float2(px, py);
+    }
+    __syncthreads();
+
+#pragma unroll
+    for (int it = 0; it < 2; ++it) {
+      int e = t + 512 * it;
+      int oct = e & 31, row = e >> 5;
+      float2 cd = crd[row];
+      float x0f = floorf(cd.x), y0f = floorf(cd.y);
+      float wx = cd.x - x0f, wy = cd.y - y0f;
+      int x0 = (int)x0f, y0i = (int)y0f;
+      int x1 = min(x0 + 1, 31), y1 = min(y0i + 1, 31);
+      float w00 = (1.f - wx) * (1.f - wy), w01 = wx * (1.f - wy);
+      float w10 = (1.f - wx) * wy,         w11 = wx * wy;
+      const float* r00 = &kvT[((size_t)(b * 1024 + y0i * 32 + x0)) * 256 + oct * 8];
+      const float* r01 = &kvT[((size_t)(b * 1024 + y0i * 32 + x1)) * 256 + oct * 8];
+      const float* r10 = &kvT[((size_t)(b * 1024 + y1 * 32 + x0)) * 256 + oct * 8];
+      const float* r11 = &kvT[((size_t)(b * 1024 + y1 * 32 + x1)) * 256 + oct * 8];
+      float4 a00 = *(const float4*)r00, b00 = *(const float4*)(r00 + 4);
+      float4 a01 = *(const float4*)r01, b01 = *(const float4*)(r01 + 4);
+      float4 a10 = *(const float4*)r10, b10 = *(const float4*)(r10 + 4);
+      float4 a11 = *(const float4*)r11, b11 = *(const float4*)(r11 + 4);
+      float v[8];
+      v[0] = a00.x * w00 + a01.x * w01 + a10.x * w10 + a11.x * w11;
+      v[1] = a00.y * w00 + a01.y * w01 + a10.y * w10 + a11.y * w11;
+      v[2] = a00.z * w00 + a01.z * w01 + a10.z * w10 + a11.z * w11;
+      v[3] = a00.w * w00 + a01.w * w01 + a10.w * w10 + a11.w * w11;
+      v[4] = b00.x * w00 + b01.x * w01 + b10.x * w10 + b11.x * w11;
+      v[5] = b00.y * w00 + b01.y * w01 + b10.y * w10 + b11.y * w11;
+      v[6] = b00.z * w00 + b01.z * w01 + b10.z * w10 + b11.z * w11;
+      v[7] = b00.w * w00 + b01.w * w01 + b10.w * w10 + b11.w * w11;
+      bf16x8 h8, l8;
+#pragma unroll
+      for (int j = 0; j < 8; ++j) {
+        unsigned short h = f2bf(v[j]);
+        h8[j] = (short)h;
+        l8[j] = (short)f2bf(v[j] - bf2f(h));
+      }
+      *(bf16x8*)&XsH[row][oct * 8] = h8;
+      *(bf16x8*)&XsL[row][oct * 8] = l8;
+    }
+    __syncthreads();
+
+    const int mat  = w >> 2;
+    const short* WAh = WH + (mat ? 131072 : 65536);
+    const short* WAl = WL + (mat ? 131072 : 65536);
+    const int om4 = (w & 3) * 4;
+
+    f32x4 acg[4][2] = {};
+#pragma unroll
+    for (int k0 = 0; k0 < 256; k0 += 32) {
+      const int k0s = k0 >> 5;
+      bf16x8 Bh[2], Bl[2];
+#pragma unroll
+      for (int nt = 0; nt < 2; ++nt) {
+        Bh[nt] = *(const bf16x8*)&XsH[nt * 16 + ln][k0 + qd * 8];
+        Bl[nt] = *(const bf16x8*)&XsL[nt * 16 + ln][k0 + qd * 8];
+      }
+#pragma unroll
+      for (int mt = 0; mt < 4; ++mt) {
+        size_t wi = ((size_t)(((om4 + mt) * 8 + k0s) * 64 + lane)) * 8;
+        bf16x8 Ah = *(const bf16x8*)&WAh[wi];
+        bf16x8 Al = *(const bf16x8*)&WAl[wi];
+#pragma unroll
+        for (int nt = 0; nt < 2; ++nt) {
+          acg[mt][nt] = __builtin_amdgcn_mfma_f32_16x16x32_bf16(Ah, Bh[nt], acg[mt][nt], 0, 0, 0);
+          acg[mt][nt] = __builtin_amdgcn_mfma_f32_16x16x32_bf16(Ah, Bl[nt], acg[mt][nt], 0, 0, 0);
+          acg[mt][nt] = __builtin_amdgcn_mfma_f32_16x16x32_bf16(Al, Bh[nt], acg[mt][nt], 0, 0, 0);
+        }
+      }
+    }
+
+#pragma unroll
+    for (int mt = 0; mt < 4; ++mt)
+#pragma unroll
+      for (int nt = 0; nt < 2; ++nt) {
+        int p  = bp0 + nt * 16 + ln;
+        int pl = p & 1023;
+        int jt = pl >> 6, jl = pl & 63;
+#pragma unroll
+        for (int i = 0; i < 4; ++i) {
+          int oc = (w & 3) * 64 + mt * 16 + qd * 4 + i;
+          unsigned short val = f2bf(acg[mt][nt][i]);
+          int bhead = b * 8 + (oc >> 5), d = oc & 31;
+          if (mat == 0) {
+            int cd2 = (d >> 3) ^ ((jl >> 2) & 3);
+            kt[((((size_t)(bhead * 16 + jt)) * 64 + jl) * 4 + cd2) * 8 + (d & 7)] = (short)val;
+          } else {
+            int jjs = ((jl & 15) << 2) | (jl >> 4);
+            int cj = (jjs >> 3) ^ (d & 7);
+            vt[((((size_t)(bhead * 16 + jt)) * 32 + d) * 8 + cj) * 8 + (jjs & 7)] = (short)val;
+          }
+        }
+      }
+  }
+  grid.sync();
+
+  {
+    auto Ks = (short (*)[2048])(SM);
+    auto Vs = (short (*)[2048])(SM + 8192);
+    auto P  = (short (*)[32][72])(SM + 16384);
+    const int b    = bid & 7;
+    const int rem2 = bid >> 3;
+    const int h    = rem2 & 7;
+    const int qp   = rem2 >> 3;
+    const int bh   = b * 8 + h;
+    const int qce  = qp + 4 * (w >> 2);
+    const int qbase = qce * 128 + (w & 3) * 16;
+
+    const short* ktb = kt + (size_t)bh * 32768;
+    const short* vtb = vt + (size_t)bh * 32768;
+
+    bf16x8 aq[2];
+    aq[0] = *(const bf16x8*)&qt[((size_t)(bh * 1024 + qbase + ln)) * 32 + qd * 8];
+    aq[1] = *(const bf16x8*)&qt[((size_t)(bh * 1024 + qbase + 64 + ln)) * 32 + qd * 8];
+
+    f32x4 acc[2][2] = {};
+    float lacc[2][4] = {};
+    const f32x4 zero = {0.f, 0.f, 0.f, 0.f};
+
+    const int sgw   = w & 3;
+    const int stoff = sgw * 512 + lane * 8;
+    const int ldoff = sgw * 512;
+
+    if (w < 4) async_copy16(&ktb[stoff], &Ks[0][ldoff]);
+    else       async_copy16(&vtb[stoff], &Vs[0][ldoff]);
+    __syncthreads();
+
+    for (int jt = 0; jt < 16; ++jt) {
+      const int cur = jt & 1, nxt = cur ^ 1;
+      if (jt < 15) {
+        if (w < 4) async_copy16(&ktb[(jt + 1) * 2048 + stoff], &Ks[nxt][ldoff]);
+        else       async_copy16(&vtb[(jt + 1) * 2048 + stoff], &Vs[nxt][ldoff]);
+      }
+
+      bf16x8 bk[4], bv[2][2];
+#pragma unroll
+      for (int kk = 0; kk < 4; ++kk)
+        bk[kk] = *(const bf16x8*)&Ks[cur][((kk * 16 + ln) * 4 + (qd ^ ((ln >> 2) & 3))) * 8];
+#pragma unroll
+      for (int kc = 0; kc < 2; ++kc)
+#pragma unroll
+        for (int ds = 0; ds < 2; ++ds)
+          bv[kc][ds] = *(const bf16x8*)&Vs[cur][((ds * 16 + ln) * 8 + ((kc * 4 + qd) ^ (ln & 7))) * 8];
+
+#pragma unroll
+      for (int qf = 0; qf < 2; ++qf) {
+        f32x4 s[4];
+        __builtin_amdgcn_s_setprio(1);
+#pragma unroll
+        for (int kk = 0; kk < 4; ++kk)
+          s[kk] = __builtin_amdgcn_mfma_f32_16x16x32_bf16(aq[qf], bk[kk], zero, 0, 0, 0);
+        __builtin_amdgcn_s_setprio(0);
+
+#pragma unroll
+        for (int i = 0; i < 4; ++i) {
+          float p0 = __builtin_amdgcn_exp2f(s[0][i]);
+          float p1 = __builtin_amdgcn_exp2f(s[1][i]);
+          float p2 = __builtin_amdgcn_exp2f(s[2][i]);
+          float p3 = __builtin_amdgcn_exp2f(s[3][i]);
+          s[0][i] = p0; s[1][i] = p1; s[2][i] = p2; s[3][i] = p3;
+          lacc[qf][i] += (p0 + p1) + (p2 + p3);
+        }
+#pragma unroll
+        for (int i = 0; i < 4; ++i) {
+          bf16x4 p4;
+#pragma unroll
+          for (int kk = 0; kk < 4; ++kk) p4[kk] = (short)f2bf_fast(s[kk][i]);
+          *(bf16x4*)&P[w][qf * 16 + qd * 4 + i][4 * ln] = p4;
+        }
+        __builtin_amdgcn_s_setprio(1);
+#pragma unroll
+        for (int kc = 0; kc < 2; ++kc) {
+          bf16x8 ap = *(const bf16x8*)&P[w][qf * 16 + ln][kc * 32 + qd * 8];
+#pragma unroll
+          for (int ds = 0; ds < 2; ++ds)
+            acc[qf][ds] = __builtin_amdgcn_mfma_f32_16x16x32_bf16(ap, bv[kc][ds], acc[qf][ds], 0, 0, 0);
+        }
+        __builtin_amdgcn_s_setprio(0);
+      }
+
+      __syncthreads();
+    }
+
+    const int bb = bh >> 3, hh2 = bh & 7;
+#pragma unroll
+    for (int qf = 0; qf < 2; ++qf)
+#pragma unroll
+      for (int i = 0; i < 4; ++i) {
+        float l = lacc[qf][i];
+        l += __shfl_xor(l, 1, 64);
+        l += __shfl_xor(l, 2, 64);
+        l += __shfl_xor(l, 4, 64);
+        l += __shfl_xor(l, 8, 64);
+        float inv = 1.f / l;
+        int qrow = qbase + qf * 64 + qd * 4 + i;
+#pragma unroll
+        for (int ds = 0; ds < 2; ++ds) {
+          float v = acc[qf][ds][i] * inv;
+          unsigned short hv = f2bf(v);
+          size_t idx = ((size_t)(bb * 1024 + qrow)) * 256 + hh2 * 32 + ds * 16 + ln;
+          bufBh[idx] = (short)hv;
+          bufBl[idx] = (short)f2bf(v - bf2f(hv));
+        }
+      }
+  }
+  grid.sync();
+
+  {
+    auto XsH = (short (*)[264])(SM);
+    auto XsL = (short (*)[264])(SM + 16896);
+    const int bp0 = bid * 32;
+    const short* Wh = WH + 196608;
+    const short* Wl = WL + 196608;
+
+#pragma unroll
+    for (int it = 0; it < 2; ++it) {
+      int e = t + 512 * it;
+      int oct = e & 31, row = e >> 5;
+      bf16x8 vh = *(const bf16x8*)&bufBh[((size_t)(bp0 + row)) * 256 + oct * 8];
+      bf16x8 vl = *(const bf16x8*)&bufBl[((size_t)(bp0 + row)) * 256 + oct * 8];
+      *(bf16x8*)&XsH[row][oct * 8] = vh;
+      *(bf16x8*)&XsL[row][oct * 8] = vl;
+    }
+    __syncthreads();
+
+    const int mh = w >> 2, ww = w & 3;
+    const int mb = mh * 8 + ww * 2;
+    f32x4 acc[2][2] = {};
+#pragma unroll
+    for (int k0 = 0; k0 < 256; k0 += 32) {
+      const int k0s = k0 >> 5;
+      bf16x8 Ah[2], Al[2], Bh[2], Bl[2];
+#pragma unroll
+      for (int mt = 0; mt < 2; ++mt) {
+        size_t wi = ((size_t)(((mb + mt) * 8 + k0s) * 64 + lane)) * 8;
+        Ah[mt] = *(const bf16x8*)&Wh[wi];
+        Al[mt] = *(const bf16x8*)&Wl[wi];
+      }
+#pragma unroll
+      for (int nt = 0; nt < 2; ++nt) {
+        Bh[nt] = *(const bf16x8*)&XsH[nt * 16 + ln][k0 + qd * 8];
+        Bl[nt] = *(const bf16x8*)&XsL[nt * 16 + ln][k0 + qd * 8];
+      }
+#pragma unroll
+      for (int mt = 0; mt < 2; ++mt)
+#pragma unroll
+        for (int nt = 0; nt < 2; ++nt) {
+          acc[mt][nt] = __builtin_amdgcn_mfma_f32_16x16x32_bf16(Ah[mt], Bh[nt], acc[mt][nt], 0, 0, 0);
+          acc[mt][nt] = __builtin_amdgcn_mfma_f32_16x16x32_bf16(Ah[mt], Bl[nt], acc[mt][nt], 0, 0, 0);
+          acc[mt][nt] = __builtin_amdgcn_mfma_f32_16x16x32_bf16(Al[mt], Bh[nt], acc[mt][nt], 0, 0, 0);
+        }
+    }
+
+    const int om = mh * 128 + ww * 32;
+#pragma unroll
+    for (int mt = 0; mt < 2; ++mt)
+#pragma unroll
+      for (int i = 0; i < 4; ++i) {
+        int o = om + mt * 16 + qd * 4 + i;
+        float bo = bout[o];
+#pragma unroll
+        for (int nt = 0; nt < 2; ++nt) {
+          int bp = bp0 + nt * 16 + ln;
+          int b = bp >> 10, p = bp & 1023;
+          out[((size_t)(b * 256 + o)) * HW_ + p] = acc[mt][nt][i] + bo;
+        }
+      }
+  }
 }
 
 extern "C" void kernel_launch(void* const* d_in, const int* in_sizes, int n_in,
@@ -639,13 +628,12 @@
   short* WL     = (short*)(base + 23 * MB);
   float* kvT    = (float*)(base + 24 * MB);
 
-  prep<<<dim3(800), dim3(256), 0, stream>>>(kv_map, Wq, Wk, Wv, Wout, Woff1,
-                                            WH, WL, wb, kvT);
-  qgemm<<<dim3(256, 2), dim3(256), 0, stream>>>(WH, WL, query_map,
-                                                qt, bufBh, bufBl);
-  convkv<<<dim3(256), dim3(512), 0, stream>>>(wb, boff1, Woff2, boff2,
-                                              bufBh, bufBl, kvT, WH, WL, kt, vt);
-  attn_mfma<<<dim3(512), dim3(256), 0, stream>>>(qt, kt, vt, bufBh, bufBl);
-  gemm_out<<<dim3(256, 2), dim3(256), 0, stream>>>(WH + 196608, WL + 196608,
-                                                   bufBh, bufBl, bout, out);
+  void* ka[] = {
+    (void*)&kv_map, (void*)&Wq, (void*)&Wk, (void*)&Wv, (void*)&Wout,
+    (void*)&Woff1, (void*)&boff1, (void*)&Woff2, (void*)&boff2,
+    (void*)&bout, (void*)&query_map, (void*)&out,
+    (void*)&WH, (void*)&WL, (void*)&wb, (void*)&kvT, (void*)&qt,
+    (void*)&kt, (void*)&vt, (void*)&bufBh, (void*)&bufBl,
+  };
+  hipLaunchCooperativeKernel((void*)mega, dim3(256), dim3(512), ka, 0, stream);
 }
```

New measurement: 302.8 us. +87.0%, slower.
